# Performance work log

Hardware: AMD Instinct MI355X
Metric: run time of the kernel (lower is better)

Reference implementation:

```python
import jax, jax.numpy as jnp
import numpy as np
from jax import lax


def _scale_config(img_sz):
    max_scale = min(img_sz)
    if max_scale > 128:
        scale = [max_scale // 16, max_scale // 8, max_scale // 4]
        weight = [0.1, 0.3, 0.6]
        dilation = [2, 2, 2]
    elif max_scale > 64:
        scale = [max_scale // 4, max_scale // 2]
        weight = [0.3, 0.7]
        dilation = [2, 2]
    else:
        scale = [max_scale // 2]
        weight = [1.0]
        dilation = [1]
    step = [max((k + 1) // 4, 1) for k in scale]
    return scale, weight, dilation, step


def _box_sum(x, k, stride, dil):
    # ones-kernel conv3d == dilated strided sliding-window sum (VALID padding)
    return lax.reduce_window(
        x, jnp.float32(0.0), lax.add,
        window_dimensions=(1, 1, k, k, k),
        window_strides=(1, 1, stride, stride, stride),
        padding='VALID',
        window_dilation=(1, 1, dil, dil, dil))


def setup_inputs() -> dict:
    key = jax.random.key(0)
    k1, k2 = jax.random.split(key)
    shape = (2, 1, 160, 160, 160)
    return {
        'input': jax.random.normal(k1, shape, dtype=jnp.float32),
        'target': jax.random.normal(k2, shape, dtype=jnp.float32),
    }


def reference(input, target):
    img_sz = input.shape[2:]
    scales, weights, dilations, steps = _scale_config(list(img_sz))
    B = input.shape[0]
    x2 = input * input
    y2 = target * target
    xy = input * target
    lncc_total = jnp.float32(0.0)
    for k, w, d, s in zip(scales, weights, dilations, steps):
        xs = _box_sum(input, k, s, d).reshape(B, -1)
        ys = _box_sum(target, k, s, d).reshape(B, -1)
        x2s = _box_sum(x2, k, s, d).reshape(B, -1)
        y2s = _box_sum(y2, k, s, d).reshape(B, -1)
        xys = _box_sum(xy, k, s, d).reshape(B, -1)
        numel = float(k ** 3)
        xm = xs / numel
        ym = ys / numel
        cross = xys - ym * xs - xm * ys + ym * xm * numel
        xvar = x2s - 2 * xm * xs + xm * xm * numel
        yvar = y2s - 2 * ym * ys + ym * ym * numel
        lncc = cross * cross / (xvar * yvar + 1e-05)
        lncc_total = lncc_total + (1.0 - lncc.mean()) * w
    return lncc_total
```

## Files before the change

### kernel.cpp

```cpp
#include <hip/hip_runtime.h>

#define DD 160

template<int N, int K, int S, int NCH, int CL>
__device__ __forceinline__ void k1_body(
    const float* __restrict__ in, const float* __restrict__ tg,
    float* __restrict__ xb, int B, long t) {
    const long XS = (long)DD * DD;
    const long P  = (long)B * XS;
    constexpr int NPC0 = (N + NCH - 1) / NCH;
    constexpr int CC   = (NPC0 + CL - 1) / CL;
    constexpr int R    = (NCH * S) / 2;
    if (t >= P * NCH * CC) return;
    long p = t % P;
    int  r = (int)(t / P);
    int chain  = r % NCH;
    int cchunk = r / NCH;
    int b = (int)(p / XS);
    long yz = p % XS;
    const float* ia = in + (long)b * DD * XS + yz;
    const float* ta = tg + (long)b * DD * XS + yz;
    const long CH = (long)B * N * XS;
    float* ob = xb + (long)b * N * XS + yz;

    const int npc = (N - chain + NCH - 1) / NCH;
    int j0 = cchunk * CL;
    if (j0 >= npc) return;
    int xp = chain + j0 * NCH;
    int x0 = xp * S;
    float s0 = 0.f, s1 = 0.f, s2 = 0.f, s3 = 0.f, s4 = 0.f;

    constexpr int G = (K >= 16) ? 8 : K;
#pragma unroll
    for (int g = 0; g < K; g += G) {
        float u[G], w[G];
#pragma unroll
        for (int j = 0; j < G; ++j)
            if (g + j < K) {
                u[j] = ia[(long)(x0 + 2 * (g + j)) * XS];
                w[j] = ta[(long)(x0 + 2 * (g + j)) * XS];
            }
#pragma unroll
        for (int j = 0; j < G; ++j)
            if (g + j < K) {
                s0 += u[j]; s1 += w[j]; s2 += u[j] * u[j];
                s3 += w[j] * w[j]; s4 += u[j] * w[j];
            }
    }
    {
        long oo = (long)xp * XS;
        ob[oo] = s0; ob[oo + CH] = s1; ob[oo + 2 * CH] = s2;
        ob[oo + 3 * CH] = s3; ob[oo + 4 * CH] = s4;
    }
#pragma unroll
    for (int q = 1; q < CL; ++q) {
        if (j0 + q >= npc) break;
        float ru[R], rw[R], au[R], aw[R];
#pragma unroll
        for (int j = 0; j < R; ++j) {
            ru[j] = ia[(long)(x0 + 2 * j) * XS];
            rw[j] = ta[(long)(x0 + 2 * j) * XS];
            au[j] = ia[(long)(x0 + 2 * K + 2 * j) * XS];
            aw[j] = ta[(long)(x0 + 2 * K + 2 * j) * XS];
        }
#pragma unroll
        for (int j = 0; j < R; ++j) {
            s0 += au[j] - ru[j];
            s1 += aw[j] - rw[j];
            s2 += au[j] * au[j] - ru[j] * ru[j];
            s3 += aw[j] * aw[j] - rw[j] * rw[j];
            s4 += au[j] * aw[j] - ru[j] * rw[j];
        }
        xp += NCH;
        x0 += NCH * S;
        long oo = (long)xp * XS;
        ob[oo] = s0; ob[oo + CH] = s1; ob[oo + 2 * CH] = s2;
        ob[oo + 3 * CH] = s3; ob[oo + 4 * CH] = s4;
    }
}

__global__ __launch_bounds__(256) void k1all(
    const float* __restrict__ in, const float* __restrict__ tg,
    float* __restrict__ xb0, float* __restrict__ xb1, float* __restrict__ xb2,
    int B, int nb2, int nb1) {
    int bid = blockIdx.x;
    if (bid < nb2) {
        k1_body<9, 40, 10, 1, 5>(in, tg, xb2, B, (long)bid * 256 + threadIdx.x);
    } else if (bid < nb2 + nb1) {
        k1_body<25, 20, 5, 2, 7>(in, tg, xb1, B, (long)(bid - nb2) * 256 + threadIdx.x);
    } else {
        k1_body<71, 10, 2, 1, 12>(in, tg, xb0, B,
                                  (long)(bid - nb2 - nb1) * 256 + threadIdx.x);
    }
}

template<int N, int K, int S>
__device__ __forceinline__ void k23_body(
    const float* __restrict__ xb, float* __restrict__ acc, int B, long row,
    float* Sw, float* wsum) {
    constexpr float numel = (float)K * K * K;
    const int tid = threadIdx.x, wid = tid >> 6, lane = tid & 63;
    const long XS = (long)DD * DD;
    const long CH = (long)B * N * XS;
    const long R3 = (long)B * N * N;
    float v = 0.f;
    if (row < R3) {
        int yp = (int)(row % N); long rr = row / N;
        int xp = (int)(rr % N);
        int b  = (int)(rr / N);
        const float* base = xb + ((long)b * N + xp) * XS + (long)(yp * S) * DD;
        const int lane2 = (lane < 32) ? lane + 128 : lane + 64;
#pragma unroll
        for (int ch = 0; ch < 5; ++ch) {
            const float* cp = base + (long)ch * CH;
            float w0 = 0.f, w1 = 0.f, w2 = 0.f;
            constexpr int G = (K > 10) ? 10 : K;
#pragma unroll
            for (int g = 0; g < K; g += G) {
                float t0[G], t1[G], t2[G];
#pragma unroll
                for (int j = 0; j < G; ++j)
                    if (g + j < K) {
                        const float* pp = cp + (long)(2 * (g + j)) * DD;
                        t0[j] = pp[lane];
                        t1[j] = pp[lane + 64];
                        t2[j] = pp[lane2];
                    }
#pragma unroll
                for (int j = 0; j < G; ++j)
                    if (g + j < K) { w0 += t0[j]; w1 += t1[j]; w2 += t2[j]; }
            }
            w2 = (lane < 32) ? w2 : 0.f;
#pragma unroll
            for (int o = 2; o <= 32; o <<= 1) {
                float q0 = __shfl_up(w0, o);
                float q1 = __shfl_up(w1, o);
                float q2 = __shfl_up(w2, o);
                if (lane >= o) { w0 += q0; w1 += q1; w2 += q2; }
            }
            float c1 = __shfl(w0, 62 + (lane & 1)); w1 += c1;
            float c2 = __shfl(w1, 62 + (lane & 1)); w2 += c2;
            float* outp = Sw + ch * 162;
            if (lane < 2) outp[lane] = 0.f;
            outp[lane + 2]  = w0;
            outp[lane + 66] = w1;
            if (lane < 32) outp[lane + 130] = w2;
        }
#pragma unroll
        for (int t = lane; t < N; t += 64) {
            int lo = t * S, hi = lo + 2 * K;
            float a0 = Sw[0 * 162 + hi] - Sw[0 * 162 + lo];
            float a1 = Sw[1 * 162 + hi] - Sw[1 * 162 + lo];
            float a2 = Sw[2 * 162 + hi] - Sw[2 * 162 + lo];
            float a3 = Sw[3 * 162 + hi] - Sw[3 * 162 + lo];
            float a4 = Sw[4 * 162 + hi] - Sw[4 * 162 + lo];
            float xm = a0 / numel, ym = a1 / numel;
            float cross = a4 - ym * a0 - xm * a1 + ym * xm * numel;
            float xvar  = a2 - 2.f * xm * a0 + xm * xm * numel;
            float yvar  = a3 - 2.f * ym * a1 + ym * ym * numel;
            v += cross * cross / (xvar * yvar + 1e-5f);
        }
    }
    for (int o = 32; o > 0; o >>= 1) v += __shfl_down(v, o, 64);
    if (lane == 0) wsum[wid] = v;
    __syncthreads();
    if (tid == 0) atomicAdd(acc, wsum[0] + wsum[1] + wsum[2] + wsum[3]);
}

__global__ __launch_bounds__(256) void k23all(
    const float* __restrict__ xb0, const float* __restrict__ xb1,
    const float* __restrict__ xb2, float* __restrict__ acc,
    int B, int b2, int b1, int b0) {
    __shared__ float Sm[4][5][162];
    __shared__ float wsum[4];
    const int wid = threadIdx.x >> 6;
    float* Sw = &Sm[wid][0][0];
    int bid = blockIdx.x;
    if (bid < b2) {
        k23_body<9, 40, 10>(xb2, acc + 2, B, (long)bid * 4 + wid, Sw, wsum);
    } else if (bid < b2 + b1) {
        k23_body<25, 20, 5>(xb1, acc + 1, B, (long)(bid - b2) * 4 + wid, Sw, wsum);
    } else {
        int local = bid - b2 - b1;
        int q = b0 >> 3, r8 = b0 & 7;
        int xcd = local & 7, idx = local >> 3;
        int swz = (xcd < r8) ? xcd * (q + 1) + idx
                             : r8 * (q + 1) + (xcd - r8) * q + idx;
        k23_body<71, 10, 2>(xb0, acc + 0, B, (long)swz * 4 + wid, Sw, wsum);
    }
}

__global__ void finalize_kernel(const float* __restrict__ acc, float* __restrict__ out,
                                float c0, float c1, float c2,
                                float w0, float w1, float w2) {
    if (threadIdx.x == 0 && blockIdx.x == 0) {
        out[0] = w0 * (1.f - acc[0] / c0) +
                 w1 * (1.f - acc[1] / c1) +
                 w2 * (1.f - acc[2] / c2);
    }
}

extern "C" void kernel_launch(void* const* d_in, const int* in_sizes, int n_in,
                              void* d_out, int out_size, void* d_ws, size_t ws_size,
                              hipStream_t stream) {
    const float* input  = (const float*)d_in[0];
    const float* target = (const float*)d_in[1];
    float* out = (float*)d_out;

    char* ws = (char*)d_ws;
    float* acc = (float*)ws;
    const size_t accPad = 256;
    const long XS = (long)DD * DD;

    const size_t fullNeed = accPad + 5ull * 2 * 105 * XS * sizeof(float);
    const int NB = (ws_size >= fullNeed) ? 2 : 1;

    float* xb0 = (float*)(ws + accPad);
    float* xb1 = xb0 + 5ull * NB * 71 * XS;
    float* xb2 = xb1 + 5ull * NB * 25 * XS;

    hipMemsetAsync(acc, 0, 3 * sizeof(float), stream);

    for (int b0i = 0; b0i < 2; b0i += NB) {
        const float* ip = input  + (size_t)b0i * DD * XS;
        const float* tp = target + (size_t)b0i * DD * XS;
        const int nb0 = 600 * NB, nb1 = 400 * NB, nb2 = 200 * NB;
        k1all<<<dim3(nb2 + nb1 + nb0), dim3(256), 0, stream>>>(
            ip, tp, xb0, xb1, xb2, NB, nb2, nb1);
        const int b2 = (NB * 81 + 3) / 4, b1 = (NB * 625 + 3) / 4,
                  b0 = (NB * 71 * 71 + 3) / 4;
        k23all<<<dim3(b2 + b1 + b0), dim3(256), 0, stream>>>(
            xb0, xb1, xb2, acc, NB, b2, b1, b0);
    }
    finalize_kernel<<<dim3(1), dim3(64), 0, stream>>>(
        acc, out,
        2.f * 71.f * 71.f * 71.f,
        2.f * 25.f * 25.f * 25.f,
        2.f * 9.f * 9.f * 9.f,
        0.1f, 0.3f, 0.6f);
}
```

Measured before the change: 166.8 us.

## Use sliding-window running sums along y in the second box-sum stage

Each wave now handles a chain of output y positions instead of one. The first position does the full K-row column sum, and each later one updates the running sums by adding the entering rows and subtracting the leaving ones. This cuts the global loads per output row from K to about 2R, and the grid shrinks to match the number of chains. In exchange there is much less parallelism (fewer waves, serial dependence within each chain), and float drift from the running add/subtract may slightly change numerics.

```diff
diff --git a/kernel.cpp b/kernel.cpp
--- a/kernel.cpp
+++ b/kernel.cpp
@@ -94,71 +94,112 @@
     }
 }
 
-template<int N, int K, int S>
-__device__ __forceinline__ void k23_body(
-    const float* __restrict__ xb, float* __restrict__ acc, int B, long row,
+template<int N, int K, int S, int NCH, int CL>
+__device__ __forceinline__ void k23c(
+    const float* __restrict__ xb, float* __restrict__ acc, int B, long task,
     float* Sw, float* wsum) {
+    constexpr int NPC0 = (N + NCH - 1) / NCH;
+    constexpr int CC   = (NPC0 + CL - 1) / CL;
+    constexpr int R    = (NCH * S) / 2;
     constexpr float numel = (float)K * K * K;
     const int tid = threadIdx.x, wid = tid >> 6, lane = tid & 63;
     const long XS = (long)DD * DD;
     const long CH = (long)B * N * XS;
-    const long R3 = (long)B * N * N;
+    const long T  = (long)B * N * NCH * CC;
     float v = 0.f;
-    if (row < R3) {
-        int yp = (int)(row % N); long rr = row / N;
-        int xp = (int)(rr % N);
-        int b  = (int)(rr / N);
-        const float* base = xb + ((long)b * N + xp) * XS + (long)(yp * S) * DD;
+    if (task < T) {
+        int chunk = (int)(task % CC); long r = task / CC;
+        int chain = (int)(r % NCH); r /= NCH;
+        int xp = (int)(r % N);
+        int b  = (int)(r / N);
+        const float* sbase = xb + ((long)b * N + xp) * XS;
         const int lane2 = (lane < 32) ? lane + 128 : lane + 64;
-#pragma unroll
-        for (int ch = 0; ch < 5; ++ch) {
-            const float* cp = base + (long)ch * CH;
-            float w0 = 0.f, w1 = 0.f, w2 = 0.f;
-            constexpr int G = (K > 10) ? 10 : K;
-#pragma unroll
-            for (int g = 0; g < K; g += G) {
-                float t0[G], t1[G], t2[G];
-#pragma unroll
-                for (int j = 0; j < G; ++j)
-                    if (g + j < K) {
-                        const float* pp = cp + (long)(2 * (g + j)) * DD;
-                        t0[j] = pp[lane];
-                        t1[j] = pp[lane + 64];
-                        t2[j] = pp[lane2];
+        float st0[5], st1[5], st2[5];
+        const int y0 = chain + chunk * CL * NCH;
+#pragma unroll
+        for (int q = 0; q < CL; ++q) {
+            int yp = y0 + q * NCH;
+            if (yp >= N) break;
+            int cb = yp * S;
+            if (q == 0) {
+#pragma unroll
+                for (int ch = 0; ch < 5; ++ch) {
+                    const float* cp = sbase + (long)ch * CH + (long)cb * DD;
+                    float a0 = 0.f, a1 = 0.f, a2 = 0.f;
+                    constexpr int G = (K > 10) ? 10 : K;
+#pragma unroll
+                    for (int g = 0; g < K; g += G) {
+                        float t0[G], t1[G], t2[G];
+#pragma unroll
+                        for (int j = 0; j < G; ++j)
+                            if (g + j < K) {
+                                const float* pp = cp + (long)(2 * (g + j)) * DD;
+                                t0[j] = pp[lane];
+                                t1[j] = pp[lane + 64];
+                                t2[j] = pp[lane2];
+                            }
+#pragma unroll
+                        for (int j = 0; j < G; ++j)
+                            if (g + j < K) { a0 += t0[j]; a1 += t1[j]; a2 += t2[j]; }
                     }
-#pragma unroll
-                for (int j = 0; j < G; ++j)
-                    if (g + j < K) { w0 += t0[j]; w1 += t1[j]; w2 += t2[j]; }
-            }
-            w2 = (lane < 32) ? w2 : 0.f;
-#pragma unroll
-            for (int o = 2; o <= 32; o <<= 1) {
-                float q0 = __shfl_up(w0, o);
-                float q1 = __shfl_up(w1, o);
-                float q2 = __shfl_up(w2, o);
-                if (lane >= o) { w0 += q0; w1 += q1; w2 += q2; }
-            }
-            float c1 = __shfl(w0, 62 + (lane & 1)); w1 += c1;
-            float c2 = __shfl(w1, 62 + (lane & 1)); w2 += c2;
-            float* outp = Sw + ch * 162;
-            if (lane < 2) outp[lane] = 0.f;
-            outp[lane + 2]  = w0;
-            outp[lane + 66] = w1;
-            if (lane < 32) outp[lane + 130] = w2;
-        }
-#pragma unroll
-        for (int t = lane; t < N; t += 64) {
-            int lo = t * S, hi = lo + 2 * K;
-            float a0 = Sw[0 * 162 + hi] - Sw[0 * 162 + lo];
-            float a1 = Sw[1 * 162 + hi] - Sw[1 * 162 + lo];
-            float a2 = Sw[2 * 162 + hi] - Sw[2 * 162 + lo];
-            float a3 = Sw[3 * 162 + hi] - Sw[3 * 162 + lo];
-            float a4 = Sw[4 * 162 + hi] - Sw[4 * 162 + lo];
-            float xm = a0 / numel, ym = a1 / numel;
-            float cross = a4 - ym * a0 - xm * a1 + ym * xm * numel;
-            float xvar  = a2 - 2.f * xm * a0 + xm * xm * numel;
-            float yvar  = a3 - 2.f * ym * a1 + ym * ym * numel;
-            v += cross * cross / (xvar * yvar + 1e-5f);
+                    st0[ch] = a0; st1[ch] = a1; st2[ch] = a2;
+                }
+            } else {
+                const int pb = cb - NCH * S;
+#pragma unroll
+                for (int ch = 0; ch < 5; ++ch) {
+                    const float* cp = sbase + (long)ch * CH;
+                    float r0[R], r1[R], r2[R], a0[R], a1[R], a2[R];
+#pragma unroll
+                    for (int j = 0; j < R; ++j) {
+                        const float* rp = cp + (long)(pb + 2 * j) * DD;
+                        const float* ap = cp + (long)(pb + 2 * K + 2 * j) * DD;
+                        r0[j] = rp[lane]; r1[j] = rp[lane + 64]; r2[j] = rp[lane2];
+                        a0[j] = ap[lane]; a1[j] = ap[lane + 64]; a2[j] = ap[lane2];
+                    }
+                    float d0 = 0.f, d1 = 0.f, d2 = 0.f;
+#pragma unroll
+                    for (int j = 0; j < R; ++j) {
+                        d0 += a0[j] - r0[j];
+                        d1 += a1[j] - r1[j];
+                        d2 += a2[j] - r2[j];
+                    }
+                    st0[ch] += d0; st1[ch] += d1; st2[ch] += d2;
+                }
+            }
+#pragma unroll
+            for (int ch = 0; ch < 5; ++ch) {
+                float v0 = st0[ch], v1 = st1[ch];
+                float v2 = (lane < 32) ? st2[ch] : 0.f;
+#pragma unroll
+                for (int o = 2; o <= 32; o <<= 1) {
+                    float q0 = __shfl_up(v0, o);
+                    float q1 = __shfl_up(v1, o);
+                    float q2 = __shfl_up(v2, o);
+                    if (lane >= o) { v0 += q0; v1 += q1; v2 += q2; }
+                }
+                float c1 = __shfl(v0, 62 + (lane & 1)); v1 += c1;
+                float c2 = __shfl(v1, 62 + (lane & 1)); v2 += c2;
+                float* outp = Sw + ch * 162;
+                if (lane < 2) outp[lane] = 0.f;
+                outp[lane + 2]  = v0;
+                outp[lane + 66] = v1;
+                if (lane < 32) outp[lane + 130] = v2;
+            }
+#pragma unroll
+            for (int t = lane; t < N; t += 64) {
+                int lo = t * S, hi = lo + 2 * K;
+                float a0 = Sw[0 * 162 + hi] - Sw[0 * 162 + lo];
+                float a1 = Sw[1 * 162 + hi] - Sw[1 * 162 + lo];
+                float a2 = Sw[2 * 162 + hi] - Sw[2 * 162 + lo];
+                float a3 = Sw[3 * 162 + hi] - Sw[3 * 162 + lo];
+                float a4 = Sw[4 * 162 + hi] - Sw[4 * 162 + lo];
+                float xm = a0 / numel, ym = a1 / numel;
+                float cross = a4 - ym * a0 - xm * a1 + ym * xm * numel;
+                float xvar  = a2 - 2.f * xm * a0 + xm * xm * numel;
+                float yvar  = a3 - 2.f * ym * a1 + ym * ym * numel;
+                v += cross * cross / (xvar * yvar + 1e-5f);
+            }
         }
     }
     for (int o = 32; o > 0; o >>= 1) v += __shfl_down(v, o, 64);
@@ -177,16 +218,16 @@
     float* Sw = &Sm[wid][0][0];
     int bid = blockIdx.x;
     if (bid < b2) {
-        k23_body<9, 40, 10>(xb2, acc + 2, B, (long)bid * 4 + wid, Sw, wsum);
+        k23c<9, 40, 10, 1, 3>(xb2, acc + 2, B, (long)bid * 4 + wid, Sw, wsum);
     } else if (bid < b2 + b1) {
-        k23_body<25, 20, 5>(xb1, acc + 1, B, (long)(bid - b2) * 4 + wid, Sw, wsum);
+        k23c<25, 20, 5, 2, 4>(xb1, acc + 1, B, (long)(bid - b2) * 4 + wid, Sw, wsum);
     } else {
         int local = bid - b2 - b1;
         int q = b0 >> 3, r8 = b0 & 7;
         int xcd = local & 7, idx = local >> 3;
         int swz = (xcd < r8) ? xcd * (q + 1) + idx
                              : r8 * (q + 1) + (xcd - r8) * q + idx;
-        k23_body<71, 10, 2>(xb0, acc + 0, B, (long)swz * 4 + wid, Sw, wsum);
+        k23c<71, 10, 2, 1, 6>(xb0, acc + 0, B, (long)swz * 4 + wid, Sw, wsum);
     }
 }
 
@@ -227,8 +268,8 @@
         const int nb0 = 600 * NB, nb1 = 400 * NB, nb2 = 200 * NB;
         k1all<<<dim3(nb2 + nb1 + nb0), dim3(256), 0, stream>>>(
             ip, tp, xb0, xb1, xb2, NB, nb2, nb1);
-        const int b2 = (NB * 81 + 3) / 4, b1 = (NB * 625 + 3) / 4,
-                  b0 = (NB * 71 * 71 + 3) / 4;
+        const int T0 = NB * 71 * 12, T1 = NB * 25 * 2 * 4, T2 = NB * 9 * 3;
+        const int b2 = (T2 + 3) / 4, b1 = (T1 + 3) / 4, b0 = (T0 + 3) / 4;
         k23all<<<dim3(b2 + b1 + b0), dim3(256), 0, stream>>>(
             xb0, xb1, xb2, acc, NB, b2, b1, b0);
     }
```

New measurement: 170.3 us. 2.1% more time.
